# Kernel optimization log

Measured on AMD Instinct MI355X. Metric: run time of the kernel, lower is better.

Reference implementation:

```python
import jax, jax.numpy as jnp
import numpy as np

B, S, D, H, FF = 2, 2048, 512, 8, 2048
DK = D // H
EPS = 1e-3  # LayerNorm epsilon from the original module


def _layer_norm(x, gamma, beta):
    # biased variance over last dim, eps added inside sqrt (matches torch var_mean unbiased=False)
    mean = jnp.mean(x, axis=-1, keepdims=True)
    var = jnp.mean(jnp.square(x - mean), axis=-1, keepdims=True)
    return gamma * ((x - mean) / jnp.sqrt(var + EPS)) + beta


def setup_inputs() -> dict:
    key = jax.random.key(0)
    ks = jax.random.split(key, 16)
    sc = 0.02
    p = {
        'x': jax.random.normal(ks[0], (B, S, D), dtype=jnp.float32),
        'lengths': jax.random.randint(ks[1], (B,), 1, S + 1, dtype=jnp.int32),
        'Wq': jax.random.normal(ks[2], (D, D), dtype=jnp.float32) * sc,
        'bq': jnp.zeros((D,), dtype=jnp.float32),
        'Wk': jax.random.normal(ks[3], (D, D), dtype=jnp.float32) * sc,
        'bk': jnp.zeros((D,), dtype=jnp.float32),
        'Wv': jax.random.normal(ks[4], (D, D), dtype=jnp.float32) * sc,
        'bv': jnp.zeros((D,), dtype=jnp.float32),
        'Wo': jax.random.normal(ks[5], (D, D), dtype=jnp.float32) * sc,
        'bo': jnp.zeros((D,), dtype=jnp.float32),
        'W1': jax.random.normal(ks[6], (D, FF), dtype=jnp.float32) * sc,
        'b1': jnp.zeros((FF,), dtype=jnp.float32),
        'W2': jax.random.normal(ks[7], (FF, D), dtype=jnp.float32) * sc,
        'b2': jnp.zeros((D,), dtype=jnp.float32),
        'gamma1': jnp.ones((D,), dtype=jnp.float32),
        'beta1': jnp.zeros((D,), dtype=jnp.float32),
        'gamma2': jnp.ones((D,), dtype=jnp.float32),
        'beta2': jnp.zeros((D,), dtype=jnp.float32),
    }
    return p


def reference(x, lengths, Wq, bq, Wk, bk, Wv, bv, Wo, bo, W1, b1, W2, b2, gamma1, beta1, gamma2, beta2):
    neg_inf = jnp.float32(-jnp.inf)
    pos = jnp.arange(S)
    # pad mask: zero out padded token embeddings (create_pad_mask)
    pad = (pos[None, :] < lengths[:, None]).astype(x.dtype)  # (B, S)
    x = x * pad[:, :, None]

    # hand-rolled multi-head attention (NO 1/sqrt(d_k) scaling, matches original)
    q = (x @ Wq + bq).reshape(B, S, H, DK)
    k = (x @ Wk + bk).reshape(B, S, H, DK)
    v = (x @ Wv + bv).reshape(B, S, H, DK)
    scores = jnp.einsum('bshd,bqhd->bhsq', q, k)  # (B, H, S_query, S_key)

    # causal mask: key col j allowed iff j <= query row i
    causal = pos[None, :] <= pos[:, None]  # (S, S)
    # padding mask: key col j allowed iff j < lengths[b]
    keep = causal[None, None, :, :] & (pos[None, None, None, :] < lengths[:, None, None, None])
    scores = jnp.where(keep, scores, neg_inf)
    attn = jax.nn.softmax(scores, axis=-1)  # (B, H, S, S)

    # FAITHFUL to torch.einsum('bhss,bshd->bshd'): repeated 's' takes the DIAGONAL
    diag = jnp.einsum('bhss->bhs', attn)  # (B, H, S)
    weighted = diag.transpose(0, 2, 1)[:, :, :, None] * v  # (B, S, H, DK)
    attn_out = weighted.reshape(B, S, D) @ Wo + bo

    x = _layer_norm(x + attn_out, gamma1, beta1)
    ff = jax.nn.relu(x @ W1 + b1) @ W2 + b2  # dropout is identity in eval
    x = _layer_norm(x + ff, gamma2, beta2)
    return x
```

## Files before the change

kernel.cpp:

```cpp
#include <hip/hip_runtime.h>

#define B_   2
#define S_   2048
#define D_   512
#define H_   8
#define DK_  64
#define FF_  2048
#define EPS_ 1e-3f
#define QS_  1536

typedef __bf16 bf16;
typedef __bf16 bf16x4 __attribute__((ext_vector_type(4)));
typedef __bf16 bf16x8 __attribute__((ext_vector_type(8)));
typedef float  f32x4  __attribute__((ext_vector_type(4)));

struct Trans4Args {
  const float* w[4];
  bf16* thi[4];
  bf16* tlo[4];
  int rowOff[4];
};

__global__ __launch_bounds__(256) void transpose4_kernel(Trans4Args a) {
  __shared__ float tl[32][33];
  const int t = threadIdx.x;
  const int tx = t & 31, ty = t >> 5;
  const int n0 = blockIdx.x * 32, k0 = blockIdx.y * 32;
  const int wsel = blockIdx.z;
  const float* __restrict__ W = a.w[wsel];
#pragma unroll
  for (int r = 0; r < 32; r += 8)
    tl[r + ty][tx] = W[(size_t)(k0 + r + ty) * 512 + n0 + tx];
  __syncthreads();
  bf16* __restrict__ Thi = a.thi[wsel];
  bf16* __restrict__ Tlo = a.tlo[wsel];
  const int ro = a.rowOff[wsel];
#pragma unroll
  for (int r = 0; r < 32; r += 8) {
    const int n = r + ty;
    const float v = tl[tx][n];
    const bf16 h = (bf16)v;
    const size_t o = (size_t)(ro + n0 + n) * 512 + k0 + tx;
    Thi[o] = h;
    Tlo[o] = (bf16)(v - (float)h);
  }
}

__global__ __launch_bounds__(256) void transpose_split_kernel(
    const float* __restrict__ W, int K, int N,
    bf16* __restrict__ Thi, bf16* __restrict__ Tlo) {
  __shared__ float tl[32][33];
  const int t = threadIdx.x;
  const int tx = t & 31, ty = t >> 5;
  const int n0 = blockIdx.x * 32, k0 = blockIdx.y * 32;
#pragma unroll
  for (int r = 0; r < 32; r += 8)
    tl[r + ty][tx] = W[(size_t)(k0 + r + ty) * N + n0 + tx];
  __syncthreads();
#pragma unroll
  for (int r = 0; r < 32; r += 8) {
    const int n = r + ty;
    const float v = tl[tx][n];
    const bf16 h = (bf16)v;
    const size_t o = (size_t)(n0 + n) * K + k0 + tx;
    Thi[o] = h;
    Tlo[o] = (bf16)(v - (float)h);
  }
}

__global__ __launch_bounds__(256) void pack_bias_kernel(const float* __restrict__ bq,
                                                        const float* __restrict__ bk,
                                                        const float* __restrict__ bv,
                                                        float* __restrict__ out) {
  const int i = blockIdx.x * 256 + threadIdx.x;
  out[i] = (i < 512) ? bq[i] : (i < 1024) ? bk[i - 512] : bv[i - 1024];
}

__global__ __launch_bounds__(256) void mask_split_kernel(const float* __restrict__ x,
                                                         const int* __restrict__ lengths,
                                                         bf16* __restrict__ xhi,
                                                         bf16* __restrict__ xlo) {
  const int idx = blockIdx.x * 256 + threadIdx.x;
  const int d4 = D_ / 4;
  const int s = (idx / d4) & (S_ - 1);
  const int b = idx / (d4 * S_);
  float4 v = reinterpret_cast<const float4*>(x)[idx];
  if (s >= lengths[b]) { v.x = 0.f; v.y = 0.f; v.z = 0.f; v.w = 0.f; }
  const float vv[4] = {v.x, v.y, v.z, v.w};
  bf16x4 h, l;
#pragma unroll
  for (int c = 0; c < 4; ++c) {
    const bf16 hh = (bf16)vv[c];
    h[c] = hh;
    l[c] = (bf16)(vv[c] - (float)hh);
  }
  reinterpret_cast<bf16x4*>(xhi)[idx] = h;
  reinterpret_cast<bf16x4*>(xlo)[idx] = l;
}

enum { EPI_BIAS = 0, EPI_BIAS_RES = 1, EPI_BIAS_RELU = 2, EPI_BIAS_RES_MASK = 3 };

template <int EPI, bool SPLIT, int BM, int BN>
__global__ __launch_bounds__(256) void gemm_kernel(
    const bf16* __restrict__ Ahi, const bf16* __restrict__ Alo,
    const bf16* __restrict__ Bhi, const bf16* __restrict__ Blo,
    const float* __restrict__ bias, const float* __restrict__ res,
    const int* __restrict__ lengths,
    float* __restrict__ C, bf16* __restrict__ Chi, bf16* __restrict__ Clo,
    int K, int ldc, int nx) {
  constexpr int MR = BM / 32, NR = BN / 32;
  __shared__ __align__(16) bf16 As[2][BM][40];
  __shared__ __align__(16) bf16 Bs[2][BN][40];
  const int t = threadIdx.x;

  const int nwg = gridDim.x;
  const int chunk = nwg >> 3;
  const int virt = (blockIdx.x & 7) * chunk + (blockIdx.x >> 3);
  const int m0 = (virt / nx) * BM, n0 = (virt % nx) * BN;

  constexpr int ATH = 256 / BM;
  constexpr int ACH = 32 / (8 * ATH);
  const int ar = t / ATH, ak = (t % ATH) * (32 / ATH);
  constexpr int BTH = 256 / BN;
  constexpr int BCH = 32 / (8 * BTH);
  const int br = t / BTH, bk = (t % BTH) * (32 / BTH);

  const int lane = t & 63, wv = t >> 6;
  const int wm = (wv >> 1) * (BM / 2), wn = (wv & 1) * (BN / 2);
  const int fr = lane & 15, fg = lane >> 4;

  f32x4 acc[MR][NR] = {};

  const bf16* pAhi = Ahi + (size_t)(m0 + ar) * K + ak;
  const bf16* pAlo = Alo + (size_t)(m0 + ar) * K + ak;
  const bf16* pBhi = Bhi + (size_t)(n0 + br) * K + bk;
  const bf16* pBlo = Blo + (size_t)(n0 + br) * K + bk;

  for (int k0 = 0; k0 < K; k0 += 32) {
#pragma unroll
    for (int c2 = 0; c2 < ACH; ++c2) {
      *reinterpret_cast<int4*>(&As[0][ar][ak + c2 * 8]) =
          *reinterpret_cast<const int4*>(pAhi + k0 + c2 * 8);
      *reinterpret_cast<int4*>(&As[1][ar][ak + c2 * 8]) =
          *reinterpret_cast<const int4*>(pAlo + k0 + c2 * 8);
    }
#pragma unroll
    for (int c2 = 0; c2 < BCH; ++c2) {
      *reinterpret_cast<int4*>(&Bs[0][br][bk + c2 * 8]) =
          *reinterpret_cast<const int4*>(pBhi + k0 + c2 * 8);
      *reinterpret_cast<int4*>(&Bs[1][br][bk + c2 * 8]) =
          *reinterpret_cast<const int4*>(pBlo + k0 + c2 * 8);
    }
    __syncthreads();

    bf16x8 ah[MR], al[MR], bh[NR], bl[NR];
#pragma unroll
    for (int m = 0; m < MR; ++m) {
      ah[m] = *reinterpret_cast<const bf16x8*>(&As[0][wm + m * 16 + fr][fg * 8]);
      al[m] = *reinterpret_cast<const bf16x8*>(&As[1][wm + m * 16 + fr][fg * 8]);
    }
#pragma unroll
    for (int n = 0; n < NR; ++n) {
      bh[n] = *reinterpret_cast<const bf16x8*>(&Bs[0][wn + n * 16 + fr][fg * 8]);
      bl[n] = *reinterpret_cast<const bf16x8*>(&Bs[1][wn + n * 16 + fr][fg * 8]);
    }
#pragma unroll
    for (int m = 0; m < MR; ++m)
#pragma unroll
      for (int n = 0; n < NR; ++n) {
        acc[m][n] = __builtin_amdgcn_mfma_f32_16x16x32_bf16(ah[m], bh[n], acc[m][n], 0, 0, 0);
        acc[m][n] = __builtin_amdgcn_mfma_f32_16x16x32_bf16(ah[m], bl[n], acc[m][n], 0, 0, 0);
        acc[m][n] = __builtin_amdgcn_mfma_f32_16x16x32_bf16(al[m], bh[n], acc[m][n], 0, 0, 0);
      }
    __syncthreads();
  }

  int lenb = 0;
  if constexpr (EPI == EPI_BIAS_RES_MASK) lenb = lengths[m0 >> 11];
  float bcol[NR];
#pragma unroll
  for (int n = 0; n < NR; ++n) bcol[n] = bias[n0 + wn + n * 16 + fr];
#pragma unroll
  for (int m = 0; m < MR; ++m)
#pragma unroll
    for (int n = 0; n < NR; ++n) {
      const int col = n0 + wn + n * 16 + fr;
#pragma unroll
      for (int r = 0; r < 4; ++r) {
        const int row = m0 + wm + m * 16 + fg * 4 + r;
        float v = acc[m][n][r] + bcol[n];
        if constexpr (EPI == EPI_BIAS_RES) v += res[(size_t)row * ldc + col];
        if constexpr (EPI == EPI_BIAS_RES_MASK) {
          const int s = row & (S_ - 1);
          if (s < lenb) v += res[(size_t)row * D_ + col];
        }
        if constexpr (EPI == EPI_BIAS_RELU) v = fmaxf(v, 0.f);
        const size_t o = (size_t)row * ldc + col;
        if constexpr (SPLIT) {
          const bf16 h = (bf16)v;
          Chi[o] = h;
          Clo[o] = (bf16)(v - (float)h);
        } else {
          C[o] = v;
        }
      }
    }
}

__global__ __launch_bounds__(256) void attn_part_kernel(const float* __restrict__ qkv,
                                                        const int* __restrict__ lengths,
                                                        float* __restrict__ pm,
                                                        float* __restrict__ pl,
                                                        float* __restrict__ pd) {
  __shared__ __align__(16) float Qs[64][68];
  __shared__ __align__(16) float Ks[64][68];
  const int t = threadIdx.x;
  const int tx = t & 15, ty = t >> 4;
  const int bh = blockIdx.y;
  const int bb = bh >> 3, h = bh & 7;

  const int p = blockIdx.x;
  int a = (int)sqrtf((float)p);
  while ((a + 1) * (a + 1) <= p) ++a;
  while (a * a > p) --a;
  int ib, jc;
  if (p >= a * a + a) { ib = 2 * a;     jc = p - (a * a + a); }
  else                { ib = 2 * a - 1; jc = p - a * a; }

  const int i0 = ib * 64;
  const int len = lengths[bb];
  if (i0 >= len || jc * 128 >= len) return;

  {
    const int r_ = t >> 4, quad = t & 15;
#pragma unroll
    for (int it = 0; it < 4; ++it) {
      const int r = it * 16 + r_;
      *reinterpret_cast<float4*>(&Qs[r][quad * 4]) = *reinterpret_cast<const float4*>(
          qkv + (size_t)(bb * S_ + i0 + r) * QS_ + h * DK_ + quad * 4);
    }
  }

  float m_r[4], l_r[4], d_r[4];
#pragma unroll
  for (int ii = 0; ii < 4; ++ii) { m_r[ii] = -1e30f; l_r[ii] = 0.f; d_r[ii] = 0.f; }

  const int jlim = min(i0 + 63, len - 1);
  for (int jt = 0; jt < 2; ++jt) {
    const int j0 = jc * 128 + jt * 64;
    if (j0 > jlim) break;
    {
      const int r_ = t >> 4, quad = t & 15;
#pragma unroll
      for (int it = 0; it < 4; ++it) {
        const int r = it * 16 + r_;
        *reinterpret_cast<float4*>(&Ks[r][quad * 4]) = *reinterpret_cast<const float4*>(
            qkv + (size_t)(bb * S_ + j0 + r) * QS_ + D_ + h * DK_ + quad * 4);
      }
    }
    __syncthreads();

    float sc[4][4] = {};
#pragma unroll 4
    for (int d0 = 0; d0 < 64; d0 += 4) {
      float4 qv[4], kv[4];
#pragma unroll
      for (int ii = 0; ii < 4; ++ii) qv[ii] = *reinterpret_cast<const float4*>(&Qs[ii * 16 + ty][d0]);
#pragma unroll
      for (int jj = 0; jj < 4; ++jj) kv[jj] = *reinterpret_cast<const float4*>(&Ks[jj * 16 + tx][d0]);
#pragma unroll
      for (int ii = 0; ii < 4; ++ii)
#pragma unroll
        for (int jj = 0; jj < 4; ++jj) {
          sc[ii][jj] = fmaf(qv[ii].x, kv[jj].x, sc[ii][jj]);
          sc[ii][jj] = fmaf(qv[ii].y, kv[jj].y, sc[ii][jj]);
          sc[ii][jj] = fmaf(qv[ii].z, kv[jj].z, sc[ii][jj]);
          sc[ii][jj] = fmaf(qv[ii].w, kv[jj].w, sc[ii][jj]);
        }
    }

#pragma unroll
    for (int ii = 0; ii < 4; ++ii) {
      const int ig = i0 + ii * 16 + ty;
      float mx = -1e30f;
#pragma unroll
      for (int jj = 0; jj < 4; ++jj) {
        const int j = j0 + jj * 16 + tx;
        if (j > ig || j >= len) sc[ii][jj] = -1e30f;
        mx = fmaxf(mx, sc[ii][jj]);
      }
#pragma unroll
      for (int off = 1; off < 16; off <<= 1) mx = fmaxf(mx, __shfl_xor(mx, off));
      const float mnew = fmaxf(m_r[ii], mx);
      float ps = 0.f, pdg = 0.f;
#pragma unroll
      for (int jj = 0; jj < 4; ++jj) {
        const int j = j0 + jj * 16 + tx;
        const float e = __expf(sc[ii][jj] - mnew);
        ps += e;
        if (j == ig) pdg = e;
      }
#pragma unroll
      for (int off = 1; off < 16; off <<= 1) {
        ps += __shfl_xor(ps, off);
        pdg += __shfl_xor(pdg, off);
      }
      const float scale = __expf(m_r[ii] - mnew);
      l_r[ii] = l_r[ii] * scale + ps;
      d_r[ii] = d_r[ii] * scale + pdg;
      m_r[ii] = mnew;
    }
    __syncthreads();
  }

  if (tx == 0) {
    const size_t base = ((size_t)(bh * 32 + ib) * 16 + jc) * 64;
#pragma unroll
    for (int ii = 0; ii < 4; ++ii) {
      const int row = ii * 16 + ty;
      const float mm = m_r[ii];
      const bool ok = mm > -1e29f;
      pm[base + row] = mm;
      pl[base + row] = ok ? l_r[ii] : 0.f;
      pd[base + row] = ok ? d_r[ii] : 0.f;
    }
  }
}

__global__ __launch_bounds__(256) void attn_merge_kernel(
    const float* __restrict__ qkv, const int* __restrict__ lengths,
    const float* __restrict__ pm, const float* __restrict__ pl,
    const float* __restrict__ pd, bf16* __restrict__ whi, bf16* __restrict__ wlo) {
  __shared__ float msh[4][64], lsh[4][64], dsh[4][64];
  __shared__ float dgs[64];
  const int t = threadIdx.x;
  const int ib = blockIdx.x, bh = blockIdx.y;
  const int bb = bh >> 3, h = bh & 7;
  const int i0 = ib * 64;
  const int len = lengths[bb];

  const int r = t & 63, g = t >> 6;
  float m = -1e30f, l = 0.f, d = 0.f;
  if (i0 < len) {
    const int jcmax = min((i0 + 63) >> 7, (len - 1) >> 7);
    const size_t base = ((size_t)(bh * 32 + ib) * 16) * 64 + r;
    for (int jc = g; jc <= jcmax; jc += 4) {
      const size_t idx = base + (size_t)jc * 64;
      const float m2 = pm[idx], l2 = pl[idx], d2 = pd[idx];
      const float mn = fmaxf(m, m2);
      const float e1 = __expf(m - mn), e2 = __expf(m2 - mn);
      l = l * e1 + l2 * e2;
      d = d * e1 + d2 * e2;
      m = mn;
    }
  }
  msh[g][r] = m; lsh[g][r] = l; dsh[g][r] = d;
  __syncthreads();
  if (t < 64) {
    float M = msh[0][t], L = lsh[0][t], Dv = dsh[0][t];
#pragma unroll
    for (int gg = 1; gg < 4; ++gg) {
      const float m2 = msh[gg][t], l2 = lsh[gg][t], d2 = dsh[gg][t];
      const float mn = fmaxf(M, m2);
      const float e1 = __expf(M - mn), e2 = __expf(m2 - mn);
      L = L * e1 + l2 * e2;
      Dv = Dv * e1 + d2 * e2;
      M = mn;
    }
    dgs[t] = (i0 + t < len) ? Dv / L : 0.f;
  }
  __syncthreads();

  const int rr = t >> 2, q = t & 3;
  const float dg = dgs[rr];
  const size_t vbase = (size_t)(bb * S_ + i0 + rr) * QS_ + 2 * D_ + h * DK_;
  const size_t obase = (size_t)(bb * S_ + i0 + rr) * D_ + h * DK_;
#pragma unroll
  for (int kk = 0; kk < 4; ++kk) {
    const int col = q * 4 + kk * 16;
    const float4 v4 = *reinterpret_cast<const float4*>(qkv + vbase + col);
    const float vv[4] = {dg * v4.x, dg * v4.y, dg * v4.z, dg * v4.w};
    bf16x4 hh, ll;
#pragma unroll
    for (int c = 0; c < 4; ++c) {
      const bf16 x = (bf16)vv[c];
      hh[c] = x;
      ll[c] = (bf16)(vv[c] - (float)x);
    }
    *reinterpret_cast<bf16x4*>(&whi[obase + col]) = hh;
    *reinterpret_cast<bf16x4*>(&wlo[obase + col]) = ll;
  }
}

template <bool SPLIT>
__global__ __launch_bounds__(256) void ln_kernel(const float* __restrict__ X,
                                                 const float* __restrict__ gamma,
                                                 const float* __restrict__ beta,
                                                 float* __restrict__ Y,
                                                 bf16* __restrict__ Yhi,
                                                 bf16* __restrict__ Ylo) {
  const int row = blockIdx.x;
  const int t = threadIdx.x;
  const float* x = X + (size_t)row * D_;
  const float2 xv = *reinterpret_cast<const float2*>(x + t * 2);
  float s = xv.x + xv.y;
  float s2 = xv.x * xv.x + xv.y * xv.y;
#pragma unroll
  for (int off = 1; off < 64; off <<= 1) {
    s += __shfl_xor(s, off);
    s2 += __shfl_xor(s2, off);
  }
  __shared__ float red[8];
  const int w = t >> 6;
  if ((t & 63) == 0) { red[w] = s; red[4 + w] = s2; }
  __syncthreads();
  const float ts  = red[0] + red[1] + red[2] + red[3];
  const float ts2 = red[4] + red[5] + red[6] + red[7];
  const float mean = ts * (1.f / D_);
  const float var  = ts2 * (1.f / D_) - mean * mean;
  const float inv  = 1.f / sqrtf(var + EPS_);
  const float2 g  = *reinterpret_cast<const float2*>(gamma + t * 2);
  const float2 bt = *reinterpret_cast<const float2*>(beta + t * 2);
  float2 o;
  o.x = g.x * ((xv.x - mean) * inv) + bt.x;
  o.y = g.y * ((xv.y - mean) * inv) + bt.y;
  *reinterpret_cast<float2*>(Y + (size_t)row * D_ + t * 2) = o;
  if constexpr (SPLIT) {
    const bf16 hx = (bf16)o.x, hy = (bf16)o.y;
    const size_t oo = (size_t)row * D_ + t * 2;
    Yhi[oo] = hx;
    Yhi[oo + 1] = hy;
    Ylo[oo] = (bf16)(o.x - (float)hx);
    Ylo[oo + 1] = (bf16)(o.y - (float)hy);
  }
}

extern "C" void kernel_launch(void* const* d_in, const int* in_sizes, int n_in,
                              void* d_out, int out_size, void* d_ws, size_t ws_size,
                              hipStream_t stream) {
  const float* x       = (const float*)d_in[0];
  const int*   lengths = (const int*)d_in[1];
  const float* Wq = (const float*)d_in[2];
  const float* bq = (const float*)d_in[3];
  const float* Wk = (const float*)d_in[4];
  const float* bk = (const float*)d_in[5];
  const float* Wv = (const float*)d_in[6];
  const float* bv = (const float*)d_in[7];
  const float* Wo = (const float*)d_in[8];
  const float* bo = (const float*)d_in[9];
  const float* W1 = (const float*)d_in[10];
  const float* b1 = (const float*)d_in[11];
  const float* W2 = (const float*)d_in[12];
  const float* b2 = (const float*)d_in[13];
  const float* gamma1 = (const float*)d_in[14];
  const float* beta1  = (const float*)d_in[15];
  const float* gamma2 = (const float*)d_in[16];
  const float* beta2  = (const float*)d_in[17];
  float* out = (float*)d_out;

  char* ws = (char*)d_ws;
  bf16*  qkvT_hi = (bf16*)(ws + 0);
  bf16*  qkvT_lo = (bf16*)(ws + 1572864);
  bf16*  WoT_hi  = (bf16*)(ws + 3145728);
  bf16*  WoT_lo  = (bf16*)(ws + 3670016);
  bf16*  W1T_hi  = (bf16*)(ws + 4194304);
  bf16*  W1T_lo  = (bf16*)(ws + 6291456);
  bf16*  W2T_hi  = (bf16*)(ws + 8388608);
  bf16*  W2T_lo  = (bf16*)(ws + 10485760);
  float* bqkv    = (float*)(ws + 12582912);
  float* qkv_f32 = (float*)(ws + 12589056);
  float* h1      = (float*)(ws + 37754880);
  float* part_m  = (float*)(ws + 37754880);
  float* part_l  = (float*)(ws + 39852032);
  float* part_d  = (float*)(ws + 41949184);
  bf16*  ff1_hi  = (bf16*)(ws + 12589056);
  bf16*  ff1_lo  = (bf16*)(ws + 29366272);
  bf16*  xm_hi   = (bf16*)(ws + 46143488);
  bf16*  xm_lo   = (bf16*)(ws + 50337792);
  bf16*  y1_hi   = (bf16*)(ws + 46143488);
  bf16*  y1_lo   = (bf16*)(ws + 50337792);
  float* h2      = (float*)(ws + 46143488);
  bf16*  wgt_hi  = (bf16*)(ws + 54532096);
  bf16*  wgt_lo  = (bf16*)(ws + 58726400);
  float* y1      = (float*)(ws + 54532096);

  const dim3 blk(256);
  const int M = B_ * S_;

  Trans4Args ta;
  ta.w[0] = Wq; ta.w[1] = Wk; ta.w[2] = Wv; ta.w[3] = Wo;
  ta.thi[0] = qkvT_hi; ta.thi[1] = qkvT_hi; ta.thi[2] = qkvT_hi; ta.thi[3] = WoT_hi;
  ta.tlo[0] = qkvT_lo; ta.tlo[1] = qkvT_lo; ta.tlo[2] = qkvT_lo; ta.tlo[3] = WoT_lo;
  ta.rowOff[0] = 0; ta.rowOff[1] = 512; ta.rowOff[2] = 1024; ta.rowOff[3] = 0;
  transpose4_kernel<<<dim3(16, 16, 4), blk, 0, stream>>>(ta);
  transpose_split_kernel<<<dim3(64, 16), blk, 0, stream>>>(W1, 512, 2048, W1T_hi, W1T_lo);
  transpose_split_kernel<<<dim3(16, 64), blk, 0, stream>>>(W2, 2048, 512, W2T_hi, W2T_lo);
  pack_bias_kernel<<<dim3(6), blk, 0, stream>>>(bq, bk, bv, bqkv);

  mask_split_kernel<<<dim3((M * D_ / 4) / 256), blk, 0, stream>>>(x, lengths, xm_hi, xm_lo);

  gemm_kernel<EPI_BIAS, false, 128, 128><<<dim3(384), blk, 0, stream>>>(
      xm_hi, xm_lo, qkvT_hi, qkvT_lo, bqkv, nullptr, nullptr,
      qkv_f32, nullptr, nullptr, 512, QS_, 12);

  attn_part_kernel<<<dim3(272, 16), blk, 0, stream>>>(qkv_f32, lengths, part_m, part_l, part_d);
  attn_merge_kernel<<<dim3(32, 16), blk, 0, stream>>>(qkv_f32, lengths, part_m, part_l, part_d,
                                                      wgt_hi, wgt_lo);

  gemm_kernel<EPI_BIAS_RES_MASK, false, 64, 64><<<dim3(512), blk, 0, stream>>>(
      wgt_hi, wgt_lo, WoT_hi, WoT_lo, bo, x, lengths,
      h1, nullptr, nullptr, 512, D_, 8);

  ln_kernel<true><<<dim3(M), blk, 0, stream>>>(h1, gamma1, beta1, y1, y1_hi, y1_lo);

  gemm_kernel<EPI_BIAS_RELU, true, 128, 128><<<dim3(512), blk, 0, stream>>>(
      y1_hi, y1_lo, W1T_hi, W1T_lo, b1, nullptr, nullptr,
      nullptr, ff1_hi, ff1_lo, 512, FF_, 16);

  gemm_kernel<EPI_BIAS_RES, false, 64, 64><<<dim3(512), blk, 0, stream>>>(
      ff1_hi, ff1_lo, W2T_hi, W2T_lo, b2, y1, nullptr,
      h2, nullptr, nullptr, FF_, D_, 8);

  ln_kernel<false><<<dim3(M), blk, 0, stream>>>(h2, gamma2, beta2, out, nullptr, nullptr);
}
```

Measured before the change: 294.4 us.

## Use 64x64 tiles everywhere, split-K the N=512 GEMMs, fold bias and residual into LayerNorm

Every GEMM now uses a fixed 64x64 tile. The QKV and FF1 GEMMs therefore launch more workgroups, and the Wo and W2 GEMMs split K in two, writing two fp32 partial buffers. The LayerNorm kernels now sum the partials, bias and residual, with masking applied inside LN1. LN2 rebuilds y1 from its hi/lo bf16 split, so the fp32 copy of y1 is no longer stored. The aim is better CU occupancy on the narrow N=512 GEMMs and fewer residual passes, at the cost of extra partial-buffer traffic and smaller tiles with less operand reuse in the big GEMMs.

Result: slower. 307.6 us (+4.5%).

```diff
diff --git a/kernel.cpp b/kernel.cpp
--- a/kernel.cpp
+++ b/kernel.cpp
@@ -98,76 +98,59 @@
   reinterpret_cast<bf16x4*>(xlo)[idx] = l;
 }
 
-enum { EPI_BIAS = 0, EPI_BIAS_RES = 1, EPI_BIAS_RELU = 2, EPI_BIAS_RES_MASK = 3 };
-
-template <int EPI, bool SPLIT, int BM, int BN>
+enum { EPI_BIAS = 0, EPI_BIAS_RELU = 2, EPI_PART = 4 };
+
+template <int EPI, bool SPLIT>
 __global__ __launch_bounds__(256) void gemm_kernel(
     const bf16* __restrict__ Ahi, const bf16* __restrict__ Alo,
     const bf16* __restrict__ Bhi, const bf16* __restrict__ Blo,
-    const float* __restrict__ bias, const float* __restrict__ res,
-    const int* __restrict__ lengths,
-    float* __restrict__ C, bf16* __restrict__ Chi, bf16* __restrict__ Clo,
-    int K, int ldc, int nx) {
-  constexpr int MR = BM / 32, NR = BN / 32;
-  __shared__ __align__(16) bf16 As[2][BM][40];
-  __shared__ __align__(16) bf16 Bs[2][BN][40];
+    const float* __restrict__ bias,
+    float* __restrict__ C, float* __restrict__ C2,
+    bf16* __restrict__ Chi, bf16* __restrict__ Clo,
+    int K, int ldc, int nx, int mn, int ksplit) {
+  __shared__ __align__(16) bf16 As[2][64][40];
+  __shared__ __align__(16) bf16 Bs[2][64][40];
   const int t = threadIdx.x;
 
   const int nwg = gridDim.x;
   const int chunk = nwg >> 3;
   const int virt = (blockIdx.x & 7) * chunk + (blockIdx.x >> 3);
-  const int m0 = (virt / nx) * BM, n0 = (virt % nx) * BN;
-
-  constexpr int ATH = 256 / BM;
-  constexpr int ACH = 32 / (8 * ATH);
-  const int ar = t / ATH, ak = (t % ATH) * (32 / ATH);
-  constexpr int BTH = 256 / BN;
-  constexpr int BCH = 32 / (8 * BTH);
-  const int br = t / BTH, bk = (t % BTH) * (32 / BTH);
-
+  const int s = virt / mn;
+  const int v2 = virt - s * mn;
+  const int m0 = (v2 / nx) * 64, n0 = (v2 % nx) * 64;
+  const int kb = s * ksplit;
+
+  const int ar = t >> 2, ak = (t & 3) * 8;
   const int lane = t & 63, wv = t >> 6;
-  const int wm = (wv >> 1) * (BM / 2), wn = (wv & 1) * (BN / 2);
+  const int wm = (wv >> 1) * 32, wn = (wv & 1) * 32;
   const int fr = lane & 15, fg = lane >> 4;
 
-  f32x4 acc[MR][NR] = {};
-
-  const bf16* pAhi = Ahi + (size_t)(m0 + ar) * K + ak;
-  const bf16* pAlo = Alo + (size_t)(m0 + ar) * K + ak;
-  const bf16* pBhi = Bhi + (size_t)(n0 + br) * K + bk;
-  const bf16* pBlo = Blo + (size_t)(n0 + br) * K + bk;
-
-  for (int k0 = 0; k0 < K; k0 += 32) {
-#pragma unroll
-    for (int c2 = 0; c2 < ACH; ++c2) {
-      *reinterpret_cast<int4*>(&As[0][ar][ak + c2 * 8]) =
-          *reinterpret_cast<const int4*>(pAhi + k0 + c2 * 8);
-      *reinterpret_cast<int4*>(&As[1][ar][ak + c2 * 8]) =
-          *reinterpret_cast<const int4*>(pAlo + k0 + c2 * 8);
-    }
-#pragma unroll
-    for (int c2 = 0; c2 < BCH; ++c2) {
-      *reinterpret_cast<int4*>(&Bs[0][br][bk + c2 * 8]) =
-          *reinterpret_cast<const int4*>(pBhi + k0 + c2 * 8);
-      *reinterpret_cast<int4*>(&Bs[1][br][bk + c2 * 8]) =
-          *reinterpret_cast<const int4*>(pBlo + k0 + c2 * 8);
-    }
+  f32x4 acc[2][2] = {};
+
+  const bf16* pAhi = Ahi + (size_t)(m0 + ar) * K + kb + ak;
+  const bf16* pAlo = Alo + (size_t)(m0 + ar) * K + kb + ak;
+  const bf16* pBhi = Bhi + (size_t)(n0 + ar) * K + kb + ak;
+  const bf16* pBlo = Blo + (size_t)(n0 + ar) * K + kb + ak;
+
+  for (int k0 = 0; k0 < ksplit; k0 += 32) {
+    *reinterpret_cast<int4*>(&As[0][ar][ak]) = *reinterpret_cast<const int4*>(pAhi + k0);
+    *reinterpret_cast<int4*>(&As[1][ar][ak]) = *reinterpret_cast<const int4*>(pAlo + k0);
+    *reinterpret_cast<int4*>(&Bs[0][ar][ak]) = *reinterpret_cast<const int4*>(pBhi + k0);
+    *reinterpret_cast<int4*>(&Bs[1][ar][ak]) = *reinterpret_cast<const int4*>(pBlo + k0);
     __syncthreads();
 
-    bf16x8 ah[MR], al[MR], bh[NR], bl[NR];
-#pragma unroll
-    for (int m = 0; m < MR; ++m) {
+    bf16x8 ah[2], al[2], bh[2], bl[2];
+#pragma unroll
+    for (int m = 0; m < 2; ++m) {
       ah[m] = *reinterpret_cast<const bf16x8*>(&As[0][wm + m * 16 + fr][fg * 8]);
       al[m] = *reinterpret_cast<const bf16x8*>(&As[1][wm + m * 16 + fr][fg * 8]);
-    }
-#pragma unroll
-    for (int n = 0; n < NR; ++n) {
-      bh[n] = *reinterpret_cast<const bf16x8*>(&Bs[0][wn + n * 16 + fr][fg * 8]);
-      bl[n] = *reinterpret_cast<const bf16x8*>(&Bs[1][wn + n * 16 + fr][fg * 8]);
-    }
-#pragma unroll
-    for (int m = 0; m < MR; ++m)
-#pragma unroll
-      for (int n = 0; n < NR; ++n) {
+      bh[m] = *reinterpret_cast<const bf16x8*>(&Bs[0][wn + m * 16 + fr][fg * 8]);
+      bl[m] = *reinterpret_cast<const bf16x8*>(&Bs[1][wn + m * 16 + fr][fg * 8]);
+    }
+#pragma unroll
+    for (int m = 0; m < 2; ++m)
+#pragma unroll
+      for (int n = 0; n < 2; ++n) {
         acc[m][n] = __builtin_amdgcn_mfma_f32_16x16x32_bf16(ah[m], bh[n], acc[m][n], 0, 0, 0);
         acc[m][n] = __builtin_amdgcn_mfma_f32_16x16x32_bf16(ah[m], bl[n], acc[m][n], 0, 0, 0);
         acc[m][n] = __builtin_amdgcn_mfma_f32_16x16x32_bf16(al[m], bh[n], acc[m][n], 0, 0, 0);
@@ -175,25 +158,21 @@
     __syncthreads();
   }
 
-  int lenb = 0;
-  if constexpr (EPI == EPI_BIAS_RES_MASK) lenb = lengths[m0 >> 11];
-  float bcol[NR];
-#pragma unroll
-  for (int n = 0; n < NR; ++n) bcol[n] = bias[n0 + wn + n * 16 + fr];
-#pragma unroll
-  for (int m = 0; m < MR; ++m)
-#pragma unroll
-    for (int n = 0; n < NR; ++n) {
+  float* __restrict__ Cw = (s == 0) ? C : C2;
+  float bcol[2] = {0.f, 0.f};
+  if constexpr (EPI != EPI_PART) {
+#pragma unroll
+    for (int n = 0; n < 2; ++n) bcol[n] = bias[n0 + wn + n * 16 + fr];
+  }
+#pragma unroll
+  for (int m = 0; m < 2; ++m)
+#pragma unroll
+    for (int n = 0; n < 2; ++n) {
       const int col = n0 + wn + n * 16 + fr;
 #pragma unroll
       for (int r = 0; r < 4; ++r) {
         const int row = m0 + wm + m * 16 + fg * 4 + r;
         float v = acc[m][n][r] + bcol[n];
-        if constexpr (EPI == EPI_BIAS_RES) v += res[(size_t)row * ldc + col];
-        if constexpr (EPI == EPI_BIAS_RES_MASK) {
-          const int s = row & (S_ - 1);
-          if (s < lenb) v += res[(size_t)row * D_ + col];
-        }
         if constexpr (EPI == EPI_BIAS_RELU) v = fmaxf(v, 0.f);
         const size_t o = (size_t)row * ldc + col;
         if constexpr (SPLIT) {
@@ -201,7 +180,7 @@
           Chi[o] = h;
           Clo[o] = (bf16)(v - (float)h);
         } else {
-          C[o] = v;
+          Cw[o] = v;
         }
       }
     }
@@ -392,19 +371,67 @@
   }
 }
 
-template <bool SPLIT>
-__global__ __launch_bounds__(256) void ln_kernel(const float* __restrict__ X,
-                                                 const float* __restrict__ gamma,
-                                                 const float* __restrict__ beta,
-                                                 float* __restrict__ Y,
-                                                 bf16* __restrict__ Yhi,
-                                                 bf16* __restrict__ Ylo) {
+__global__ __launch_bounds__(256) void ln1_fused_kernel(
+    const float* __restrict__ P0, const float* __restrict__ P1,
+    const float* __restrict__ x, const int* __restrict__ lengths,
+    const float* __restrict__ bo,
+    const float* __restrict__ gamma, const float* __restrict__ beta,
+    bf16* __restrict__ Yhi, bf16* __restrict__ Ylo) {
   const int row = blockIdx.x;
   const int t = threadIdx.x;
-  const float* x = X + (size_t)row * D_;
-  const float2 xv = *reinterpret_cast<const float2*>(x + t * 2);
-  float s = xv.x + xv.y;
-  float s2 = xv.x * xv.x + xv.y * xv.y;
+  const int lenb = lengths[row >> 11];
+  const bool valid = (row & (S_ - 1)) < lenb;
+  const size_t ro = (size_t)row * D_ + t * 2;
+  const float2 p0 = *reinterpret_cast<const float2*>(P0 + ro);
+  const float2 p1 = *reinterpret_cast<const float2*>(P1 + ro);
+  const float2 xv = *reinterpret_cast<const float2*>(x + ro);
+  const float2 bv = *reinterpret_cast<const float2*>(bo + t * 2);
+  float hx = p0.x + p1.x + bv.x + (valid ? xv.x : 0.f);
+  float hy = p0.y + p1.y + bv.y + (valid ? xv.y : 0.f);
+
+  float s = hx + hy, s2 = hx * hx + hy * hy;
+#pragma unroll
+  for (int off = 1; off < 64; off <<= 1) {
+    s += __shfl_xor(s, off);
+    s2 += __shfl_xor(s2, off);
+  }
+  __shared__ float red[8];
+  const int w = t >> 6;
+  if ((t & 63) == 0) { red[w] = s; red[4 + w] = s2; }
+  __syncthreads();
+  const float ts  = red[0] + red[1] + red[2] + red[3];
+  const float ts2 = red[4] + red[5] + red[6] + red[7];
+  const float mean = ts * (1.f / D_);
+  const float var  = ts2 * (1.f / D_) - mean * mean;
+  const float inv  = 1.f / sqrtf(var + EPS_);
+  const float2 g  = *reinterpret_cast<const float2*>(gamma + t * 2);
+  const float2 bt = *reinterpret_cast<const float2*>(beta + t * 2);
+  const float ox = g.x * ((hx - mean) * inv) + bt.x;
+  const float oy = g.y * ((hy - mean) * inv) + bt.y;
+  const bf16 ohx = (bf16)ox, ohy = (bf16)oy;
+  Yhi[ro] = ohx;  Yhi[ro + 1] = ohy;
+  Ylo[ro] = (bf16)(ox - (float)ohx);
+  Ylo[ro + 1] = (bf16)(oy - (float)ohy);
+}
+
+__global__ __launch_bounds__(256) void ln2_fused_kernel(
+    const float* __restrict__ Q0, const float* __restrict__ Q1,
+    const bf16* __restrict__ Yhi, const bf16* __restrict__ Ylo,
+    const float* __restrict__ b2,
+    const float* __restrict__ gamma, const float* __restrict__ beta,
+    float* __restrict__ out) {
+  const int row = blockIdx.x;
+  const int t = threadIdx.x;
+  const size_t ro = (size_t)row * D_ + t * 2;
+  const float2 q0 = *reinterpret_cast<const float2*>(Q0 + ro);
+  const float2 q1 = *reinterpret_cast<const float2*>(Q1 + ro);
+  const float2 bv = *reinterpret_cast<const float2*>(b2 + t * 2);
+  const float y1x = (float)Yhi[ro] + (float)Ylo[ro];
+  const float y1y = (float)Yhi[ro + 1] + (float)Ylo[ro + 1];
+  float hx = q0.x + q1.x + bv.x + y1x;
+  float hy = q0.y + q1.y + bv.y + y1y;
+
+  float s = hx + hy, s2 = hx * hx + hy * hy;
 #pragma unroll
   for (int off = 1; off < 64; off <<= 1) {
     s += __shfl_xor(s, off);
@@ -422,17 +449,9 @@
   const float2 g  = *reinterpret_cast<const float2*>(gamma + t * 2);
   const float2 bt = *reinterpret_cast<const float2*>(beta + t * 2);
   float2 o;
-  o.x = g.x * ((xv.x - mean) * inv) + bt.x;
-  o.y = g.y * ((xv.y - mean) * inv) + bt.y;
-  *reinterpret_cast<float2*>(Y + (size_t)row * D_ + t * 2) = o;
-  if constexpr (SPLIT) {
-    const bf16 hx = (bf16)o.x, hy = (bf16)o.y;
-    const size_t oo = (size_t)row * D_ + t * 2;
-    Yhi[oo] = hx;
-    Yhi[oo + 1] = hy;
-    Ylo[oo] = (bf16)(o.x - (float)hx);
-    Ylo[oo + 1] = (bf16)(o.y - (float)hy);
-  }
+  o.x = g.x * ((hx - mean) * inv) + bt.x;
+  o.y = g.y * ((hy - mean) * inv) + bt.y;
+  *reinterpret_cast<float2*>(out + ro) = o;
 }
 
 extern "C" void kernel_launch(void* const* d_in, const int* in_sizes, int n_in,
@@ -469,7 +488,8 @@
   bf16*  W2T_lo  = (bf16*)(ws + 10485760);
   float* bqkv    = (float*)(ws + 12582912);
   float* qkv_f32 = (float*)(ws + 12589056);
-  float* h1      = (float*)(ws + 37754880);
+  float* P0      = (float*)(ws + 12589056);
+  float* P1      = (float*)(ws + 20977664);
   float* part_m  = (float*)(ws + 37754880);
   float* part_l  = (float*)(ws + 39852032);
   float* part_d  = (float*)(ws + 41949184);
@@ -479,10 +499,10 @@
   bf16*  xm_lo   = (bf16*)(ws + 50337792);
   bf16*  y1_hi   = (bf16*)(ws + 46143488);
   bf16*  y1_lo   = (bf16*)(ws + 50337792);
-  float* h2      = (float*)(ws + 46143488);
   bf16*  wgt_hi  = (bf16*)(ws + 54532096);
   bf16*  wgt_lo  = (bf16*)(ws + 58726400);
-  float* y1      = (float*)(ws + 54532096);
+  float* Q0      = (float*)(ws + 54532096);
+  float* Q1      = (float*)(ws + 0);
 
   const dim3 blk(256);
   const int M = B_ * S_;
@@ -499,27 +519,29 @@
 
   mask_split_kernel<<<dim3((M * D_ / 4) / 256), blk, 0, stream>>>(x, lengths, xm_hi, xm_lo);
 
-  gemm_kernel<EPI_BIAS, false, 128, 128><<<dim3(384), blk, 0, stream>>>(
-      xm_hi, xm_lo, qkvT_hi, qkvT_lo, bqkv, nullptr, nullptr,
-      qkv_f32, nullptr, nullptr, 512, QS_, 12);
+  gemm_kernel<EPI_BIAS, false><<<dim3(1536), blk, 0, stream>>>(
+      xm_hi, xm_lo, qkvT_hi, qkvT_lo, bqkv,
+      qkv_f32, nullptr, nullptr, nullptr, 512, QS_, 24, 1536, 512);
 
   attn_part_kernel<<<dim3(272, 16), blk, 0, stream>>>(qkv_f32, lengths, part_m, part_l, part_d);
   attn_merge_kernel<<<dim3(32, 16), blk, 0, stream>>>(qkv_f32, lengths, part_m, part_l, part_d,
                                                       wgt_hi, wgt_lo);
 
-  gemm_kernel<EPI_BIAS_RES_MASK, false, 64, 64><<<dim3(512), blk, 0, stream>>>(
-      wgt_hi, wgt_lo, WoT_hi, WoT_lo, bo, x, lengths,
-      h1, nullptr, nullptr, 512, D_, 8);
-
-  ln_kernel<true><<<dim3(M), blk, 0, stream>>>(h1, gamma1, beta1, y1, y1_hi, y1_lo);
-
-  gemm_kernel<EPI_BIAS_RELU, true, 128, 128><<<dim3(512), blk, 0, stream>>>(
-      y1_hi, y1_lo, W1T_hi, W1T_lo, b1, nullptr, nullptr,
-      nullptr, ff1_hi, ff1_lo, 512, FF_, 16);
-
-  gemm_kernel<EPI_BIAS_RES, false, 64, 64><<<dim3(512), blk, 0, stream>>>(
-      ff1_hi, ff1_lo, W2T_hi, W2T_lo, b2, y1, nullptr,
-      h2, nullptr, nullptr, FF_, D_, 8);
-
-  ln_kernel<false><<<dim3(M), blk, 0, stream>>>(h2, gamma2, beta2, out, nullptr, nullptr);
-}
+  gemm_kernel<EPI_PART, false><<<dim3(1024), blk, 0, stream>>>(
+      wgt_hi, wgt_lo, WoT_hi, WoT_lo, nullptr,
+      P0, P1, nullptr, nullptr, 512, D_, 8, 512, 256);
+
+  ln1_fused_kernel<<<dim3(M), blk, 0, stream>>>(P0, P1, x, lengths, bo,
+                                                gamma1, beta1, y1_hi, y1_lo);
+
+  gemm_kernel<EPI_BIAS_RELU, true><<<dim3(2048), blk, 0, stream>>>(
+      y1_hi, y1_lo, W1T_hi, W1T_lo, b1,
+      nullptr, nullptr, ff1_hi, ff1_lo, 512, FF_, 32, 2048, 512);
+
+  gemm_kernel<EPI_PART, false><<<dim3(1024), blk, 0, stream>>>(
+      ff1_hi, ff1_lo, W2T_hi, W2T_lo, nullptr,
+      Q0, Q1, nullptr, nullptr, FF_, D_, 8, 512, 1024);
+
+  ln2_fused_kernel<<<dim3(M), blk, 0, stream>>>(Q0, Q1, y1_hi, y1_lo, b2,
+                                                gamma2, beta2, out);
+}
```
